# Kernel tuning notes

Hardware: AMD Instinct MI355X
Metric: run time of the kernel (lower is better)

Reference implementation:

```python
import jax, jax.numpy as jnp
import numpy as np

NUM_EMBEDDINGS = 1024
DIM = 256
COMMIT = 0.25


def setup_inputs() -> dict:
    key = jax.random.key(0)
    k_inp, k_emb = jax.random.split(key)
    inp = jax.random.normal(k_inp, (64, 1024, DIM), dtype=jnp.float32)
    # emb.weight.data.uniform_(-1/num_embeddings, 1/num_embeddings)
    emb = jax.random.uniform(
        k_emb, (NUM_EMBEDDINGS, DIM), dtype=jnp.float32,
        minval=-1.0 / NUM_EMBEDDINGS, maxval=1.0 / NUM_EMBEDDINGS)
    return {"inp": inp, "emb": emb}


def reference(inp, emb):
    flat = inp.reshape(-1, DIM)                       # [N, D]
    d = (jnp.sum(flat * flat, axis=1, keepdims=True)
         + jnp.sum(emb * emb, axis=1)
         - 2.0 * flat @ emb.T)
    idx = jnp.argmin(d, axis=1)                       # [N]
    # gather instead of one-hot matmul (same math)
    quant = emb[idx].reshape(inp.shape)               # [B, T, D]
    codebook_loss = jnp.mean((jax.lax.stop_gradient(quant) - inp) ** 2)
    commit_loss = jnp.mean((quant - jax.lax.stop_gradient(inp)) ** 2)
    loss = codebook_loss + COMMIT * commit_loss
    st = inp + jax.lax.stop_gradient(quant - inp)     # straight-through
    return st, loss, idx
```

## Files before the change

kernel.cpp:

```cpp
#include <hip/hip_runtime.h>
#include <math.h>

#define D 256
#define K 1024
#define NR 65536
#define ST_SIZE (NR * D)
#define LOSS_OFF ST_SIZE
#define IDX_OFF (ST_SIZE + 1)
#define BM 64
#define TPB 256
#define NRND 32
#define NBLK (NR / BM)
#define MARGIN 2e-3f
#define CAND_CAP 2048

typedef short bf16x8 __attribute__((ext_vector_type(8)));
typedef float f32x4 __attribute__((ext_vector_type(4)));

#define GLDS(g, s) __builtin_amdgcn_global_load_lds( \
    (const __attribute__((address_space(1))) unsigned int*)(g), \
    (__attribute__((address_space(3))) unsigned int*)(s), 16, 0, 0)

__device__ __forceinline__ unsigned f2bf(float f) {
    unsigned u = __float_as_uint(f);
    return (u + 0x7FFFu + ((u >> 16) & 1u)) >> 16;
}
__device__ __forceinline__ uint4 packB(float4 a, float4 b) {
    uint4 w;
    w.x = f2bf(-2.f * a.x) | (f2bf(-2.f * a.y) << 16);
    w.y = f2bf(-2.f * a.z) | (f2bf(-2.f * a.w) << 16);
    w.z = f2bf(-2.f * b.x) | (f2bf(-2.f * b.y) << 16);
    w.w = f2bf(-2.f * b.z) | (f2bf(-2.f * b.w) << 16);
    return w;
}

__device__ __forceinline__ float sq_nf(float x) {
    float s = x * x;
    asm volatile("" : "+v"(s));
    return s;
}
template <typename F>
__device__ __forceinline__ float np_sumsq256(F ld) {
    float tot[2];
    #pragma unroll
    for (int h = 0; h < 2; ++h) {
        const int base = h * 128;
        float r[8];
        #pragma unroll
        for (int j = 0; j < 8; ++j) r[j] = sq_nf(ld(base + j));
        for (int i = 8; i < 128; i += 8) {
            #pragma unroll
            for (int j = 0; j < 8; ++j) r[j] += sq_nf(ld(base + i + j));
        }
        tot[h] = ((r[0] + r[1]) + (r[2] + r[3])) + ((r[4] + r[5]) + (r[6] + r[7]));
    }
    return tot[0] + tot[1];
}

__global__ void prep_kernel(const float* __restrict__ emb,
                            unsigned short* __restrict__ pb,
                            float* __restrict__ se) {
    if (blockIdx.x < 128) {
        const int c  = blockIdx.x * 256 + threadIdx.x;
        const int ct = c >> 9;
        const int r  = c & 511;
        const int kb = r >> 6, l = r & 63;
        const float* srcp = emb + (size_t)(ct * 16 + (l & 15)) * D
                                + kb * 32 + (l >> 4) * 8;
        const float4* s4 = (const float4*)srcp;
        ((uint4*)pb)[c] = packB(s4[0], s4[1]);
    } else {
        const int k = (blockIdx.x - 128) * 256 + threadIdx.x;
        const float* row = emb + (size_t)k * D;
        se[k] = np_sumsq256([&](int i) { return row[i]; });
    }
}

__global__ __attribute__((amdgpu_waves_per_eu(2, 4))) __launch_bounds__(TPB)
void vq_main(const float* __restrict__ inp, const float* __restrict__ emb,
             const unsigned short* __restrict__ pb, const float* __restrict__ se,
             float* __restrict__ out, double* __restrict__ lsum) {
    __shared__ __align__(16) unsigned short Bt[2][8192];
    __shared__ float se_s[K];
    __shared__ float sx_s[BM];
    __shared__ float rfin[BM];
    __shared__ unsigned cand[CAND_CAP];
    __shared__ float candsc[CAND_CAP];
    __shared__ unsigned bestd[BM];
    __shared__ unsigned bestc[BM];
    __shared__ int ncand;

    const int t   = threadIdx.x;
    const int ws  = t >> 6;
    const int l   = t & 63;
    const int c16 = l & 15;
    const int g4  = l >> 4;
    const int r0  = blockIdx.x * BM;

    #pragma unroll
    for (int i = 0; i < K / TPB; ++i) se_s[i * TPB + t] = se[i * TPB + t];
    if (t < BM) { bestd[t] = 0xFFFFFFFFu; bestc[t] = 0xFFFFFFFFu; }
    if (t == 0) ncand = 0;

    bf16x8 afr[8];
    {
        const float* xrow = inp + (size_t)(r0 + ws * 16 + c16) * D;
        #pragma unroll
        for (int kb = 0; kb < 8; ++kb) {
            const float4* p4 = (const float4*)(xrow + kb * 32 + g4 * 8);
            float4 a = p4[0], b = p4[1];
            bf16x8 v;
            v[0] = (short)f2bf(a.x); v[1] = (short)f2bf(a.y);
            v[2] = (short)f2bf(a.z); v[3] = (short)f2bf(a.w);
            v[4] = (short)f2bf(b.x); v[5] = (short)f2bf(b.y);
            v[6] = (short)f2bf(b.z); v[7] = (short)f2bf(b.w);
            afr[kb] = v;
        }
    }

    {
        const int slot = t & 15, grp = t >> 4;
        const int j = slot & 7, h = slot >> 3;
        #pragma unroll
        for (int p = 0; p < 4; ++p) {
            const int row = p * 16 + grp;
            const float* base = inp + (size_t)(r0 + row) * D + h * 128 + j;
            float s = sq_nf(base[0]);
            #pragma unroll
            for (int i = 1; i < 16; ++i) s += sq_nf(base[i * 8]);
            #pragma unroll
            for (int m = 1; m <= 8; m <<= 1) s += __shfl_xor(s, m);
            if (slot == 0) sx_s[row] = s;
        }
    }

    float rmin[4];
    #pragma unroll
    for (int i = 0; i < 4; ++i) rmin[i] = INFINITY;

    const uint4* srcv = (const uint4*)pb;

    auto stage = [&](int buf, int cr) {
        const uint4* g = srcv + (size_t)cr * 1024;
        #pragma unroll
        for (int q = 0; q < 4; ++q) {
            char* lbase = (char*)&Bt[buf][0] + (q * 256 + ws * 64) * 16;
            GLDS(g + q * TPB + t, lbase);
        }
    };

    stage(0, 0);
    int cur = 0;
    for (int cr = 0; cr < NRND; ++cr) {
        __syncthreads();
        if (cr + 1 < NRND) stage(cur ^ 1, cr + 1);
        const bf16x8* bch = (const bf16x8*)&Bt[cur][0];
        f32x4 acc0, acc1;
        {
            const float sev0 = se_s[(cr * 2 + 0) * 16 + c16];
            const float sev1 = se_s[(cr * 2 + 1) * 16 + c16];
            #pragma unroll
            for (int i = 0; i < 4; ++i) { acc0[i] = sev0; acc1[i] = sev1; }
        }
        #pragma unroll
        for (int kb = 0; kb < 8; ++kb) {
            acc0 = __builtin_amdgcn_mfma_f32_16x16x32_bf16(afr[kb], bch[kb * 64 + l],       acc0, 0, 0, 0);
            acc1 = __builtin_amdgcn_mfma_f32_16x16x32_bf16(afr[kb], bch[512 + kb * 64 + l], acc1, 0, 0, 0);
        }

        #pragma unroll
        for (int i = 0; i < 4; ++i) rmin[i] = fminf(rmin[i], fminf(acc0[i], acc1[i]));
        if ((cr & 1) == 0) {
            #pragma unroll
            for (int i = 0; i < 4; ++i) {
                #pragma unroll
                for (int m = 1; m <= 8; m <<= 1)
                    rmin[i] = fminf(rmin[i], __shfl_xor(rmin[i], m));
            }
        }
        #pragma unroll
        for (int i = 0; i < 4; ++i) {
            const int row_local = ws * 16 + g4 * 4 + i;
            if (acc0[i] <= rmin[i] + MARGIN) {
                const int p = atomicAdd(&ncand, 1);
                if (p < CAND_CAP) {
                    cand[p]   = ((unsigned)row_local << 10) | (unsigned)((cr * 2) * 16 + c16);
                    candsc[p] = acc0[i];
                }
            }
            if (acc1[i] <= rmin[i] + MARGIN) {
                const int p = atomicAdd(&ncand, 1);
                if (p < CAND_CAP) {
                    cand[p]   = ((unsigned)row_local << 10) | (unsigned)((cr * 2 + 1) * 16 + c16);
                    candsc[p] = acc1[i];
                }
            }
        }
        cur ^= 1;
    }
    #pragma unroll
    for (int i = 0; i < 4; ++i) {
        #pragma unroll
        for (int m = 1; m <= 8; m <<= 1)
            rmin[i] = fminf(rmin[i], __shfl_xor(rmin[i], m));
    }
    if (c16 == 0) {
        #pragma unroll
        for (int i = 0; i < 4; ++i)
            rfin[ws * 16 + g4 * 4 + i] = rmin[i];
    }
    __syncthreads();

    int n = ncand; if (n > CAND_CAP) n = CAND_CAP;
    {
        const int qw = l >> 4, lq = l & 15;
        for (int ci = ws * 4 + qw; ci < n; ci += 16) {
            const unsigned uc = cand[ci];
            const int row_local = uc >> 10, code = uc & 1023;
            const float sc = candsc[ci];
            if (sc <= rfin[row_local] + MARGIN) {
                const float4* xp = (const float4*)(inp + (size_t)(r0 + row_local) * D) + lq * 4;
                const float4* ep = (const float4*)(emb + (size_t)code * D) + lq * 4;
                float p = 0.f;
                #pragma unroll
                for (int q = 0; q < 4; ++q) {
                    float4 x = xp[q], e = ep[q];
                    p = fmaf(x.x, e.x, p);
                    p = fmaf(x.y, e.y, p);
                    p = fmaf(x.z, e.z, p);
                    p = fmaf(x.w, e.w, p);
                }
                #pragma unroll
                for (int m = 1; m <= 8; m <<= 1) p += __shfl_xor(p, m);
                const float tv = sx_s[row_local] + se_s[code];
                const float d  = fmaf(-2.f, p, tv);
                if (lq == 0) {
                    candsc[ci] = d;
                    atomicMin(&bestd[row_local], __float_as_uint(d));
                }
            } else if (lq == 0) {
                candsc[ci] = INFINITY;
            }
        }
    }
    __syncthreads();
    for (int ci = t; ci < n; ci += TPB) {
        const unsigned uc = cand[ci];
        if (__float_as_uint(candsc[ci]) == bestd[uc >> 10])
            atomicMin(&bestc[uc >> 10], uc & 1023u);
    }
    __syncthreads();
    if (t < BM) out[IDX_OFF + r0 + t] = (float)bestc[t];

    {
        float4* out4 = (float4*)(out + (size_t)r0 * D);
        const float4* emb4 = (const float4*)emb;
        #pragma unroll
        for (int i = 0; i < (BM * D) / (4 * TPB); ++i) {
            const int e = i * TPB + t;
            out4[e] = emb4[((size_t)bestc[e >> 6] << 6) + (e & 63)];
        }
    }

    if (t < 64) {
        double s = (double)__uint_as_float(bestd[t]);
        #pragma unroll
        for (int m = 1; m < 64; m <<= 1) s += __shfl_xor(s, m);
        if (t == 0) lsum[blockIdx.x] = s;
    }
}

__global__ void fin_kernel(const double* __restrict__ lsum, float* __restrict__ out) {
    const int l = threadIdx.x;
    double s = 0.0;
    #pragma unroll
    for (int i = 0; i < NBLK / 64; ++i) s += lsum[l * (NBLK / 64) + i];
    #pragma unroll
    for (int m = 1; m < 64; m <<= 1) s += __shfl_xor(s, m);
    if (l == 0) out[LOSS_OFF] = (float)(1.25 * s / (double)ST_SIZE);
}

extern "C" void kernel_launch(void* const* d_in, const int* in_sizes, int n_in,
                              void* d_out, int out_size, void* d_ws, size_t ws_size,
                              hipStream_t stream) {
    const float* inp = (const float*)d_in[0];
    const float* emb = (const float*)d_in[1];
    float* out = (float*)d_out;
    unsigned short* pb = (unsigned short*)d_ws;
    float*  se_ws      = (float*)((char*)d_ws + 524288);
    double* lsum       = (double*)((char*)d_ws + 528384);

    prep_kernel<<<132, 256, 0, stream>>>(emb, pb, se_ws);
    vq_main<<<NBLK, TPB, 0, stream>>>(inp, emb, pb, se_ws, out, lsum);
    fin_kernel<<<1, 64, 0, stream>>>(lsum, out);
}
```

Before: 174.1 us.

## Halve codebook tile per round and drop shared se cache to cut LDS

Each main-loop round now processes 16 codes instead of 32, doubling the round count and halving the double-buffered B tile in LDS. The shared copy of code norms is removed and norms are read from global memory instead, and the candidate buffer is shrunk. The aim is to lower LDS use per block so more blocks fit per CU. In exchange there are twice as many barriers and rounds, less MFMA work between syncs, and more min-reduction overhead. A smaller candidate cap also raises the risk of overflow.

```diff
diff --git a/kernel.cpp b/kernel.cpp
--- a/kernel.cpp
+++ b/kernel.cpp
@@ -9,10 +9,10 @@
 #define IDX_OFF (ST_SIZE + 1)
 #define BM 64
 #define TPB 256
-#define NRND 32
+#define NRND 64
 #define NBLK (NR / BM)
 #define MARGIN 2e-3f
-#define CAND_CAP 2048
+#define CAND_CAP 1536
 
 typedef short bf16x8 __attribute__((ext_vector_type(8)));
 typedef float f32x4 __attribute__((ext_vector_type(4)));
@@ -80,8 +80,7 @@
 void vq_main(const float* __restrict__ inp, const float* __restrict__ emb,
              const unsigned short* __restrict__ pb, const float* __restrict__ se,
              float* __restrict__ out, double* __restrict__ lsum) {
-    __shared__ __align__(16) unsigned short Bt[2][8192];
-    __shared__ float se_s[K];
+    __shared__ __align__(16) unsigned short Bt[2][4096];
     __shared__ float sx_s[BM];
     __shared__ float rfin[BM];
     __shared__ unsigned cand[CAND_CAP];
@@ -97,8 +96,6 @@
     const int g4  = l >> 4;
     const int r0  = blockIdx.x * BM;
 
-    #pragma unroll
-    for (int i = 0; i < K / TPB; ++i) se_s[i * TPB + t] = se[i * TPB + t];
     if (t < BM) { bestd[t] = 0xFFFFFFFFu; bestc[t] = 0xFFFFFFFFu; }
     if (t == 0) ncand = 0;
 
@@ -141,9 +138,9 @@
     const uint4* srcv = (const uint4*)pb;
 
     auto stage = [&](int buf, int cr) {
-        const uint4* g = srcv + (size_t)cr * 1024;
-        #pragma unroll
-        for (int q = 0; q < 4; ++q) {
+        const uint4* g = srcv + (size_t)cr * 512;
+        #pragma unroll
+        for (int q = 0; q < 2; ++q) {
             char* lbase = (char*)&Bt[buf][0] + (q * 256 + ws * 64) * 16;
             GLDS(g + q * TPB + t, lbase);
         }
@@ -155,21 +152,18 @@
         __syncthreads();
         if (cr + 1 < NRND) stage(cur ^ 1, cr + 1);
         const bf16x8* bch = (const bf16x8*)&Bt[cur][0];
-        f32x4 acc0, acc1;
+        f32x4 acc;
         {
-            const float sev0 = se_s[(cr * 2 + 0) * 16 + c16];
-            const float sev1 = se_s[(cr * 2 + 1) * 16 + c16];
-            #pragma unroll
-            for (int i = 0; i < 4; ++i) { acc0[i] = sev0; acc1[i] = sev1; }
-        }
-        #pragma unroll
-        for (int kb = 0; kb < 8; ++kb) {
-            acc0 = __builtin_amdgcn_mfma_f32_16x16x32_bf16(afr[kb], bch[kb * 64 + l],       acc0, 0, 0, 0);
-            acc1 = __builtin_amdgcn_mfma_f32_16x16x32_bf16(afr[kb], bch[512 + kb * 64 + l], acc1, 0, 0, 0);
-        }
-
-        #pragma unroll
-        for (int i = 0; i < 4; ++i) rmin[i] = fminf(rmin[i], fminf(acc0[i], acc1[i]));
+            const float sev = se[cr * 16 + c16];
+            #pragma unroll
+            for (int i = 0; i < 4; ++i) acc[i] = sev;
+        }
+        #pragma unroll
+        for (int kb = 0; kb < 8; ++kb)
+            acc = __builtin_amdgcn_mfma_f32_16x16x32_bf16(afr[kb], bch[kb * 64 + l], acc, 0, 0, 0);
+
+        #pragma unroll
+        for (int i = 0; i < 4; ++i) rmin[i] = fminf(rmin[i], acc[i]);
         if ((cr & 1) == 0) {
             #pragma unroll
             for (int i = 0; i < 4; ++i) {
@@ -180,19 +174,12 @@
         }
         #pragma unroll
         for (int i = 0; i < 4; ++i) {
-            const int row_local = ws * 16 + g4 * 4 + i;
-            if (acc0[i] <= rmin[i] + MARGIN) {
+            if (acc[i] <= rmin[i] + MARGIN) {
+                const int row_local = ws * 16 + g4 * 4 + i;
                 const int p = atomicAdd(&ncand, 1);
                 if (p < CAND_CAP) {
-                    cand[p]   = ((unsigned)row_local << 10) | (unsigned)((cr * 2) * 16 + c16);
-                    candsc[p] = acc0[i];
-                }
-            }
-            if (acc1[i] <= rmin[i] + MARGIN) {
-                const int p = atomicAdd(&ncand, 1);
-                if (p < CAND_CAP) {
-                    cand[p]   = ((unsigned)row_local << 10) | (unsigned)((cr * 2 + 1) * 16 + c16);
-                    candsc[p] = acc1[i];
+                    cand[p]   = ((unsigned)row_local << 10) | (unsigned)(cr * 16 + c16);
+                    candsc[p] = acc[i];
                 }
             }
         }
@@ -232,7 +219,7 @@
                 }
                 #pragma unroll
                 for (int m = 1; m <= 8; m <<= 1) p += __shfl_xor(p, m);
-                const float tv = sx_s[row_local] + se_s[code];
+                const float tv = sx_s[row_local] + se[code];
                 const float d  = fmaf(-2.f, p, tv);
                 if (lq == 0) {
                     candsc[ci] = d;
```

Result: faster. 157.3 us (-9.7%).

## Double rows per block to 128 with 512 threads, split MFMA accumulators, drop LDS se

Applied to the files above, without the earlier changes.

Doubles the row tile per block to 128 rows with 512 threads (8 waves), so each staged codebook chunk in LDS is reused by twice as many rows and the number of blocks halves. The MFMA chain is split into even/odd accumulators to shorten the dependency chain, and the per-block copy of codebook norms into LDS is removed in favor of direct global reads. This costs more registers and threads per block and raises the candidate buffer capacity, at the risk of lower occupancy and extra global loads inside the main loop.

```diff
diff --git a/kernel.cpp b/kernel.cpp
--- a/kernel.cpp
+++ b/kernel.cpp
@@ -7,12 +7,12 @@
 #define ST_SIZE (NR * D)
 #define LOSS_OFF ST_SIZE
 #define IDX_OFF (ST_SIZE + 1)
-#define BM 64
-#define TPB 256
+#define BM 128
+#define TPB 512
 #define NRND 32
 #define NBLK (NR / BM)
 #define MARGIN 2e-3f
-#define CAND_CAP 2048
+#define CAND_CAP 3072
 
 typedef short bf16x8 __attribute__((ext_vector_type(8)));
 typedef float f32x4 __attribute__((ext_vector_type(4)));
@@ -81,7 +81,6 @@
              const unsigned short* __restrict__ pb, const float* __restrict__ se,
              float* __restrict__ out, double* __restrict__ lsum) {
     __shared__ __align__(16) unsigned short Bt[2][8192];
-    __shared__ float se_s[K];
     __shared__ float sx_s[BM];
     __shared__ float rfin[BM];
     __shared__ unsigned cand[CAND_CAP];
@@ -97,8 +96,6 @@
     const int g4  = l >> 4;
     const int r0  = blockIdx.x * BM;
 
-    #pragma unroll
-    for (int i = 0; i < K / TPB; ++i) se_s[i * TPB + t] = se[i * TPB + t];
     if (t < BM) { bestd[t] = 0xFFFFFFFFu; bestc[t] = 0xFFFFFFFFu; }
     if (t == 0) ncand = 0;
 
@@ -123,7 +120,7 @@
         const int j = slot & 7, h = slot >> 3;
         #pragma unroll
         for (int p = 0; p < 4; ++p) {
-            const int row = p * 16 + grp;
+            const int row = p * 32 + grp;
             const float* base = inp + (size_t)(r0 + row) * D + h * 128 + j;
             float s = sq_nf(base[0]);
             #pragma unroll
@@ -143,8 +140,8 @@
     auto stage = [&](int buf, int cr) {
         const uint4* g = srcv + (size_t)cr * 1024;
         #pragma unroll
-        for (int q = 0; q < 4; ++q) {
-            char* lbase = (char*)&Bt[buf][0] + (q * 256 + ws * 64) * 16;
+        for (int q = 0; q < 2; ++q) {
+            char* lbase = (char*)&Bt[buf][0] + (q * 512 + ws * 64) * 16;
             GLDS(g + q * TPB + t, lbase);
         }
     };
@@ -155,21 +152,26 @@
         __syncthreads();
         if (cr + 1 < NRND) stage(cur ^ 1, cr + 1);
         const bf16x8* bch = (const bf16x8*)&Bt[cur][0];
-        f32x4 acc0, acc1;
+        f32x4 a0e, a0o, a1e, a1o;
         {
-            const float sev0 = se_s[(cr * 2 + 0) * 16 + c16];
-            const float sev1 = se_s[(cr * 2 + 1) * 16 + c16];
-            #pragma unroll
-            for (int i = 0; i < 4; ++i) { acc0[i] = sev0; acc1[i] = sev1; }
-        }
-        #pragma unroll
-        for (int kb = 0; kb < 8; ++kb) {
-            acc0 = __builtin_amdgcn_mfma_f32_16x16x32_bf16(afr[kb], bch[kb * 64 + l],       acc0, 0, 0, 0);
-            acc1 = __builtin_amdgcn_mfma_f32_16x16x32_bf16(afr[kb], bch[512 + kb * 64 + l], acc1, 0, 0, 0);
-        }
-
-        #pragma unroll
-        for (int i = 0; i < 4; ++i) rmin[i] = fminf(rmin[i], fminf(acc0[i], acc1[i]));
+            const float sev0 = se[(cr * 2 + 0) * 16 + c16];
+            const float sev1 = se[(cr * 2 + 1) * 16 + c16];
+            #pragma unroll
+            for (int i = 0; i < 4; ++i) { a0e[i] = sev0; a0o[i] = 0.f; a1e[i] = sev1; a1o[i] = 0.f; }
+        }
+        #pragma unroll
+        for (int kb = 0; kb < 8; kb += 2) {
+            a0e = __builtin_amdgcn_mfma_f32_16x16x32_bf16(afr[kb],     bch[kb * 64 + l],             a0e, 0, 0, 0);
+            a1e = __builtin_amdgcn_mfma_f32_16x16x32_bf16(afr[kb],     bch[512 + kb * 64 + l],       a1e, 0, 0, 0);
+            a0o = __builtin_amdgcn_mfma_f32_16x16x32_bf16(afr[kb + 1], bch[(kb + 1) * 64 + l],       a0o, 0, 0, 0);
+            a1o = __builtin_amdgcn_mfma_f32_16x16x32_bf16(afr[kb + 1], bch[512 + (kb + 1) * 64 + l], a1o, 0, 0, 0);
+        }
+        float sc0[4], sc1[4];
+        #pragma unroll
+        for (int i = 0; i < 4; ++i) { sc0[i] = a0e[i] + a0o[i]; sc1[i] = a1e[i] + a1o[i]; }
+
+        #pragma unroll
+        for (int i = 0; i < 4; ++i) rmin[i] = fminf(rmin[i], fminf(sc0[i], sc1[i]));
         if ((cr & 1) == 0) {
             #pragma unroll
             for (int i = 0; i < 4; ++i) {
@@ -181,18 +183,18 @@
         #pragma unroll
         for (int i = 0; i < 4; ++i) {
             const int row_local = ws * 16 + g4 * 4 + i;
-            if (acc0[i] <= rmin[i] + MARGIN) {
+            if (sc0[i] <= rmin[i] + MARGIN) {
                 const int p = atomicAdd(&ncand, 1);
                 if (p < CAND_CAP) {
                     cand[p]   = ((unsigned)row_local << 10) | (unsigned)((cr * 2) * 16 + c16);
-                    candsc[p] = acc0[i];
-                }
-            }
-            if (acc1[i] <= rmin[i] + MARGIN) {
+                    candsc[p] = sc0[i];
+                }
+            }
+            if (sc1[i] <= rmin[i] + MARGIN) {
                 const int p = atomicAdd(&ncand, 1);
                 if (p < CAND_CAP) {
                     cand[p]   = ((unsigned)row_local << 10) | (unsigned)((cr * 2 + 1) * 16 + c16);
-                    candsc[p] = acc1[i];
+                    candsc[p] = sc1[i];
                 }
             }
         }
@@ -214,7 +216,7 @@
     int n = ncand; if (n > CAND_CAP) n = CAND_CAP;
     {
         const int qw = l >> 4, lq = l & 15;
-        for (int ci = ws * 4 + qw; ci < n; ci += 16) {
+        for (int ci = ws * 4 + qw; ci < n; ci += 32) {
             const unsigned uc = cand[ci];
             const int row_local = uc >> 10, code = uc & 1023;
             const float sc = candsc[ci];
@@ -232,7 +234,7 @@
                 }
                 #pragma unroll
                 for (int m = 1; m <= 8; m <<= 1) p += __shfl_xor(p, m);
-                const float tv = sx_s[row_local] + se_s[code];
+                const float tv = sx_s[row_local] + se[code];
                 const float d  = fmaf(-2.f, p, tv);
                 if (lq == 0) {
                     candsc[ci] = d;
@@ -263,7 +265,7 @@
     }
 
     if (t < 64) {
-        double s = (double)__uint_as_float(bestd[t]);
+        double s = (double)__uint_as_float(bestd[t]) + (double)__uint_as_float(bestd[t + 64]);
         #pragma unroll
         for (int m = 1; m < 64; m <<= 1) s += __shfl_xor(s, m);
         if (t == 0) lsum[blockIdx.x] = s;
```

Result: faster. 142.1 us, median of 2 (-18.4%).
